# Performance work log

Hardware: AMD Instinct MI355X
Metric: run time of the kernel (lower is better)

The kernel has to match this reference:

```python
import jax, jax.numpy as jnp
import numpy as np

NUM_HEADS = 12
WIN = 7  # window_size[0] == window_size[1]


def setup_inputs() -> dict:
    key = jax.random.key(0)
    ks = jax.random.split(key, 8)
    B_, N, C = 2048, WIN * WIN, 384
    nW = 64
    return {
        "x": jax.random.normal(ks[0], (B_, N, C), dtype=jnp.float32),
        "mask": jax.random.normal(ks[1], (nW, N, N), dtype=jnp.float32),
        "qkv_w": jax.random.normal(ks[2], (3 * C, C), dtype=jnp.float32) * 0.02,
        "qkv_b": jax.random.normal(ks[3], (3 * C,), dtype=jnp.float32) * 0.02,
        "proj_w": jax.random.normal(ks[4], (C, C), dtype=jnp.float32) * 0.02,
        "proj_b": jax.random.normal(ks[5], (C,), dtype=jnp.float32) * 0.02,
        "rpb_table": jax.random.normal(ks[6], ((2 * WIN - 1) ** 2, NUM_HEADS), dtype=jnp.float32) * 0.02,
        "rel_index": jax.random.randint(ks[7], (N * N,), 0, (2 * WIN - 1) ** 2, dtype=jnp.int32),
    }


def reference(x, mask, qkv_w, qkv_b, proj_w, proj_b, rpb_table, rel_index):
    B_, N, C = x.shape
    H = NUM_HEADS
    d = C // H
    scale = d ** -0.5

    # QKV projection (quant wrappers act as identity in non-quant state)
    qkv = x @ qkv_w.T + qkv_b                      # [B_, N, 3C]
    qkv = qkv.reshape(B_, N, 3, H, d).transpose(2, 0, 3, 1, 4)  # [3, B_, H, N, d]
    q, k, v = qkv[0], qkv[1], qkv[2]

    attn = jnp.einsum("bhnd,bhmd->bhnm", q * scale, k)  # [B_, H, N, N]

    # relative position bias gather: [N*N] -> [N, N, H] -> [H, N, N]
    bias = rpb_table[rel_index].reshape(N, N, H).transpose(2, 0, 1)
    attn = attn + bias[None]

    # shifted-window mask add
    nW = mask.shape[0]
    attn = attn.reshape(B_ // nW, nW, H, N, N) + mask[None, :, None]
    attn = attn.reshape(B_, H, N, N)

    attn = jax.nn.softmax(attn, axis=-1)

    out = jnp.einsum("bhnm,bhmd->bhnd", attn, v)   # [B_, H, N, d]
    out = out.transpose(0, 2, 1, 3).reshape(B_, N, C)
    out = out @ proj_w.T + proj_b
    return out, attn
```

## Files before the change

kernel.cpp:

```cpp
#include <hip/hip_runtime.h>
#include <hip/hip_bf16.h>
#include <stdint.h>

#define H_ 12
#define D_ 32
#define N_ 49
#define C_ 384
#define B_TOT 2048
#define BH 24576
#define M_ROWS 100352
#define SCALE 0.17677669529663689f

typedef float f32x4 __attribute__((ext_vector_type(4)));
typedef __bf16 bf16x8 __attribute__((ext_vector_type(8)));
typedef unsigned short ushortx8 __attribute__((ext_vector_type(8)));

static __device__ __forceinline__ unsigned short f2bf(float f) {
  __bf16 b = (__bf16)f;
  return __builtin_bit_cast(unsigned short, b);
}

__global__ void cast_bf16(const float* __restrict__ in,
                          unsigned short* __restrict__ out, int n8) {
  int i = blockIdx.x * blockDim.x + threadIdx.x;
  const int stride = gridDim.x * blockDim.x;
  for (; i < n8; i += stride) {
    float4 a = ((const float4*)in)[2 * i];
    float4 b = ((const float4*)in)[2 * i + 1];
    ushortx8 v;
    v[0] = f2bf(a.x); v[1] = f2bf(a.y); v[2] = f2bf(a.z); v[3] = f2bf(a.w);
    v[4] = f2bf(b.x); v[5] = f2bf(b.y); v[6] = f2bf(b.z); v[7] = f2bf(b.w);
    *(ushortx8*)&out[(size_t)i * 8] = v;
  }
}

__global__ void build_comb(const float* __restrict__ mask,
                           const float* __restrict__ rpb,
                           const int* __restrict__ ridx,
                           float* __restrict__ comb) {
  const int h = blockIdx.x, w = blockIdx.y;
  float* cb = comb + (size_t)(w * H_ + h) * 4096;
  const float* mw = mask + (size_t)w * N_ * N_;
  for (int e = threadIdx.x; e < 4096; e += 256) {
    const int r = e >> 6, c = e & 63;
    float v;
    if (c >= N_) v = -1e30f;
    else if (r >= N_) v = 0.0f;
    else v = mw[r * N_ + c] + rpb[ridx[r * N_ + c] * H_ + h];
    cb[e] = v;
  }
}

__global__ __launch_bounds__(256, 3)
void qkv_gemm(const unsigned short* __restrict__ A,
              const unsigned short* __restrict__ W,
              const float* __restrict__ bias, unsigned short* __restrict__ qkv) {
  __shared__ unsigned short lA[2][128 * 40];
  __shared__ unsigned short lB[2][128 * 40];
  const int tid = threadIdx.x;
  const int bn = blockIdx.x, bm = blockIdx.y;
  const int lane = tid & 63, wv = tid >> 6;
  const int wm = wv >> 1, wn = wv & 1;
  const int lo = lane & 15, hi = lane >> 4;
  const int r0 = tid >> 2, r1 = r0 + 64;
  const int off = (tid & 3) * 8;

  const unsigned short* Ab = A + (size_t)bm * 128 * 384;
  const unsigned short* Wb = W + (size_t)bn * 128 * 384;

  f32x4 acc[4][4];
#pragma unroll
  for (int i = 0; i < 4; i++)
#pragma unroll
    for (int j = 0; j < 4; j++)
#pragma unroll
      for (int r = 0; r < 4; r++) acc[i][j][r] = 0.0f;

  *(uint4*)&lA[0][r0 * 40 + off] = *(const uint4*)(Ab + r0 * 384 + off);
  *(uint4*)&lA[0][r1 * 40 + off] = *(const uint4*)(Ab + r1 * 384 + off);
  *(uint4*)&lB[0][r0 * 40 + off] = *(const uint4*)(Wb + r0 * 384 + off);
  *(uint4*)&lB[0][r1 * 40 + off] = *(const uint4*)(Wb + r1 * 384 + off);
  __syncthreads();

  int buf = 0;
  for (int kt = 0; kt < 12; kt++) {
    uint4 pa0, pa1, pb0, pb1;
    if (kt < 11) {
      const int kc = (kt + 1) * 32 + off;
      pa0 = *(const uint4*)(Ab + r0 * 384 + kc);
      pa1 = *(const uint4*)(Ab + r1 * 384 + kc);
      pb0 = *(const uint4*)(Wb + r0 * 384 + kc);
      pb1 = *(const uint4*)(Wb + r1 * 384 + kc);
    }
    bf16x8 af[4], bfm[4];
#pragma unroll
    for (int mt = 0; mt < 4; mt++)
      af[mt] = *(const bf16x8*)&lA[buf][(wm * 64 + mt * 16 + lo) * 40 + hi * 8];
#pragma unroll
    for (int nt = 0; nt < 4; nt++)
      bfm[nt] = *(const bf16x8*)&lB[buf][(wn * 64 + nt * 16 + lo) * 40 + hi * 8];
#pragma unroll
    for (int mt = 0; mt < 4; mt++)
#pragma unroll
      for (int nt = 0; nt < 4; nt++)
        acc[mt][nt] = __builtin_amdgcn_mfma_f32_16x16x32_bf16(af[mt], bfm[nt], acc[mt][nt], 0, 0, 0);
    if (kt < 11) {
      *(uint4*)&lA[buf ^ 1][r0 * 40 + off] = pa0;
      *(uint4*)&lA[buf ^ 1][r1 * 40 + off] = pa1;
      *(uint4*)&lB[buf ^ 1][r0 * 40 + off] = pb0;
      *(uint4*)&lB[buf ^ 1][r1 * 40 + off] = pb1;
    }
    __syncthreads();
    buf ^= 1;
  }

#pragma unroll
  for (int nt = 0; nt < 4; nt++) {
    const int j = bn * 128 + wn * 64 + nt * 16 + lo;
    const float bj = bias[j];
    const int which = j / 384;
    const int rem = j - which * 384;
    const int h = rem >> 5, dd = rem & 31;
    const float mul = (which == 0) ? SCALE : 1.0f;
#pragma unroll
    for (int mt = 0; mt < 4; mt++) {
#pragma unroll
      for (int r = 0; r < 4; r++) {
        const int i = bm * 128 + wm * 64 + mt * 16 + hi * 4 + r;
        const int b = i / 49, sq = i - b * 49;
        const float val = (acc[mt][nt][r] + bj) * mul;
        qkv[((size_t)which * BH + (size_t)b * H_ + h) * (N_ * D_) + sq * D_ + dd] = f2bf(val);
      }
    }
  }
}

__global__ __launch_bounds__(64, 2)
void attn_kernel(const unsigned short* __restrict__ qkv,
                 const float* __restrict__ comb,
                 float* __restrict__ probs,
                 unsigned short* __restrict__ av) {
  __shared__ unsigned short P[64 * 72];
  __shared__ unsigned short VT[32 * 72];
  const int lane = threadIdx.x;
  const int lo = lane & 15, hi = lane >> 4;
  const int h = blockIdx.x, b = blockIdx.y;

  const unsigned short* qp = qkv + (size_t)(b * H_ + h) * (N_ * D_);
  const unsigned short* kp = qp + (size_t)BH * (N_ * D_);
  const unsigned short* vp = kp + (size_t)BH * (N_ * D_);

  {
    unsigned int* vz = (unsigned int*)VT;
#pragma unroll
    for (int i = 0; i < 18; i++) vz[lane + 64 * i] = 0u;
  }
  __syncthreads();

  bf16x8 aq[4], bk[4];
#pragma unroll
  for (int t = 0; t < 4; t++) {
    aq[t] = *(const bf16x8*)(qp + (t * 16 + lo) * D_ + hi * 8);
    bk[t] = *(const bf16x8*)(kp + (t * 16 + lo) * D_ + hi * 8);
  }
  f32x4 s[4][4];
#pragma unroll
  for (int mt = 0; mt < 4; mt++)
#pragma unroll
    for (int nt = 0; nt < 4; nt++) {
#pragma unroll
      for (int r = 0; r < 4; r++) s[mt][nt][r] = 0.0f;
      s[mt][nt] = __builtin_amdgcn_mfma_f32_16x16x32_bf16(aq[mt], bk[nt], s[mt][nt], 0, 0, 0);
    }

#pragma unroll
  for (int it = 0; it < 4; it++) {
    const int idx = it * 64 + lane;
    if (idx < 196) {
      const int sq = idx >> 2, ch = idx & 3;
      ushortx8 vv = *(const ushortx8*)(vp + sq * D_ + ch * 8);
#pragma unroll
      for (int jj = 0; jj < 8; jj++) VT[(ch * 8 + jj) * 72 + sq] = vv[jj];
    }
  }

  const float* cb = comb + (size_t)((b & 63) * H_ + h) * 4096;
#pragma unroll
  for (int mt = 0; mt < 4; mt++) {
#pragma unroll
    for (int r = 0; r < 4; r++) {
      const int row = mt * 16 + hi * 4 + r;
      const float* crow = cb + row * 64 + lo;
      float v0 = s[mt][0][r] + crow[0];
      float v1 = s[mt][1][r] + crow[16];
      float v2 = s[mt][2][r] + crow[32];
      float v3 = s[mt][3][r] + crow[48];
      float m = fmaxf(fmaxf(v0, v1), fmaxf(v2, v3));
      m = fmaxf(m, __shfl_xor(m, 1));
      m = fmaxf(m, __shfl_xor(m, 2));
      m = fmaxf(m, __shfl_xor(m, 4));
      m = fmaxf(m, __shfl_xor(m, 8));
      v0 = __expf(v0 - m); v1 = __expf(v1 - m);
      v2 = __expf(v2 - m); v3 = __expf(v3 - m);
      float sum = v0 + v1 + v2 + v3;
      sum += __shfl_xor(sum, 1);
      sum += __shfl_xor(sum, 2);
      sum += __shfl_xor(sum, 4);
      sum += __shfl_xor(sum, 8);
      const float rinv = 1.0f / sum;
      s[mt][0][r] = v0 * rinv; s[mt][1][r] = v1 * rinv;
      s[mt][2][r] = v2 * rinv; s[mt][3][r] = v3 * rinv;
    }
  }

  const size_t pbase = (size_t)(b * H_ + h) * N_ * N_;
#pragma unroll
  for (int mt = 0; mt < 4; mt++) {
#pragma unroll
    for (int r = 0; r < 4; r++) {
      const int row = mt * 16 + hi * 4 + r;
      if (row < N_) {
#pragma unroll
        for (int nt = 0; nt < 4; nt++) {
          const int c = nt * 16 + lo;
          if (c < N_) probs[pbase + row * N_ + c] = s[mt][nt][r];
        }
      }
#pragma unroll
      for (int nt = 0; nt < 4; nt++)
        P[row * 72 + nt * 16 + lo] = f2bf(s[mt][nt][r]);
    }
  }
  __syncthreads();

  f32x4 o[4][2];
#pragma unroll
  for (int mt = 0; mt < 4; mt++)
#pragma unroll
    for (int n2 = 0; n2 < 2; n2++)
#pragma unroll
      for (int r = 0; r < 4; r++) o[mt][n2][r] = 0.0f;
#pragma unroll
  for (int ks = 0; ks < 2; ks++) {
    bf16x8 pa[4], vb[2];
#pragma unroll
    for (int mt = 0; mt < 4; mt++)
      pa[mt] = *(const bf16x8*)&P[(mt * 16 + lo) * 72 + ks * 32 + hi * 8];
#pragma unroll
    for (int n2 = 0; n2 < 2; n2++)
      vb[n2] = *(const bf16x8*)&VT[(n2 * 16 + lo) * 72 + ks * 32 + hi * 8];
#pragma unroll
    for (int mt = 0; mt < 4; mt++)
#pragma unroll
      for (int n2 = 0; n2 < 2; n2++)
        o[mt][n2] = __builtin_amdgcn_mfma_f32_16x16x32_bf16(pa[mt], vb[n2], o[mt][n2], 0, 0, 0);
  }

#pragma unroll
  for (int mt = 0; mt < 4; mt++) {
#pragma unroll
    for (int r = 0; r < 4; r++) {
      const int row = mt * 16 + hi * 4 + r;
      if (row < N_) {
#pragma unroll
        for (int n2 = 0; n2 < 2; n2++) {
          const int dv = n2 * 16 + lo;
          av[((size_t)b * N_ + row) * C_ + h * D_ + dv] = f2bf(o[mt][n2][r]);
        }
      }
    }
  }
}

__global__ __launch_bounds__(256, 3)
void proj_gemm(const unsigned short* __restrict__ A,
               const unsigned short* __restrict__ W,
               const float* __restrict__ bias, float* __restrict__ out) {
  __shared__ unsigned short lA[2][128 * 40];
  __shared__ unsigned short lB[2][128 * 40];
  const int tid = threadIdx.x;
  const int bn = blockIdx.x, bm = blockIdx.y;
  const int lane = tid & 63, wv = tid >> 6;
  const int wm = wv >> 1, wn = wv & 1;
  const int lo = lane & 15, hi = lane >> 4;
  const int r0 = tid >> 2, r1 = r0 + 64;
  const int off = (tid & 3) * 8;

  const unsigned short* Ab = A + (size_t)bm * 128 * 384;
  const unsigned short* Wb = W + (size_t)bn * 128 * 384;

  f32x4 acc[4][4];
#pragma unroll
  for (int i = 0; i < 4; i++)
#pragma unroll
    for (int j = 0; j < 4; j++)
#pragma unroll
      for (int r = 0; r < 4; r++) acc[i][j][r] = 0.0f;

  *(uint4*)&lA[0][r0 * 40 + off] = *(const uint4*)(Ab + r0 * 384 + off);
  *(uint4*)&lA[0][r1 * 40 + off] = *(const uint4*)(Ab + r1 * 384 + off);
  *(uint4*)&lB[0][r0 * 40 + off] = *(const uint4*)(Wb + r0 * 384 + off);
  *(uint4*)&lB[0][r1 * 40 + off] = *(const uint4*)(Wb + r1 * 384 + off);
  __syncthreads();

  int buf = 0;
  for (int kt = 0; kt < 12; kt++) {
    uint4 pa0, pa1, pb0, pb1;
    if (kt < 11) {
      const int kc = (kt + 1) * 32 + off;
      pa0 = *(const uint4*)(Ab + r0 * 384 + kc);
      pa1 = *(const uint4*)(Ab + r1 * 384 + kc);
      pb0 = *(const uint4*)(Wb + r0 * 384 + kc);
      pb1 = *(const uint4*)(Wb + r1 * 384 + kc);
    }
    bf16x8 af[4], bfm[4];
#pragma unroll
    for (int mt = 0; mt < 4; mt++)
      af[mt] = *(const bf16x8*)&lA[buf][(wm * 64 + mt * 16 + lo) * 40 + hi * 8];
#pragma unroll
    for (int nt = 0; nt < 4; nt++)
      bfm[nt] = *(const bf16x8*)&lB[buf][(wn * 64 + nt * 16 + lo) * 40 + hi * 8];
#pragma unroll
    for (int mt = 0; mt < 4; mt++)
#pragma unroll
      for (int nt = 0; nt < 4; nt++)
        acc[mt][nt] = __builtin_amdgcn_mfma_f32_16x16x32_bf16(af[mt], bfm[nt], acc[mt][nt], 0, 0, 0);
    if (kt < 11) {
      *(uint4*)&lA[buf ^ 1][r0 * 40 + off] = pa0;
      *(uint4*)&lA[buf ^ 1][r1 * 40 + off] = pa1;
      *(uint4*)&lB[buf ^ 1][r0 * 40 + off] = pb0;
      *(uint4*)&lB[buf ^ 1][r1 * 40 + off] = pb1;
    }
    __syncthreads();
    buf ^= 1;
  }

#pragma unroll
  for (int nt = 0; nt < 4; nt++) {
    const int j = bn * 128 + wn * 64 + nt * 16 + lo;
    const float bj = bias[j];
#pragma unroll
    for (int mt = 0; mt < 4; mt++) {
#pragma unroll
      for (int r = 0; r < 4; r++) {
        const int i = bm * 128 + wm * 64 + mt * 16 + hi * 4 + r;
        out[(size_t)i * 384 + j] = acc[mt][nt][r] + bj;
      }
    }
  }
}

extern "C" void kernel_launch(void* const* d_in, const int* in_sizes, int n_in,
                              void* d_out, int out_size, void* d_ws, size_t ws_size,
                              hipStream_t stream) {
  const float* x      = (const float*)d_in[0];
  const float* mask   = (const float*)d_in[1];
  const float* qkv_w  = (const float*)d_in[2];
  const float* qkv_b  = (const float*)d_in[3];
  const float* proj_w = (const float*)d_in[4];
  const float* proj_b = (const float*)d_in[5];
  const float* rpb    = (const float*)d_in[6];
  const int*   ridx   = (const int*)d_in[7];

  unsigned short* qkv   = (unsigned short*)d_ws;
  unsigned short* av    = qkv + (size_t)3 * BH * N_ * D_;
  unsigned short* x_bf  = av;
  float* comb           = (float*)(av + (size_t)M_ROWS * C_);
  unsigned short* wq_bf = (unsigned short*)(comb + 768 * 4096);
  unsigned short* wp_bf = wq_bf + 1152 * 384;
  float* out   = (float*)d_out;
  float* probs = out + (size_t)M_ROWS * C_;

  cast_bf16<<<2048, 256, 0, stream>>>(x, x_bf, M_ROWS * C_ / 8);
  cast_bf16<<<216, 256, 0, stream>>>(qkv_w, wq_bf, 1152 * 384 / 8);
  cast_bf16<<<72, 256, 0, stream>>>(proj_w, wp_bf, 384 * 384 / 8);
  build_comb<<<dim3(H_, 64), 256, 0, stream>>>(mask, rpb, ridx, comb);
  qkv_gemm<<<dim3(9, 784), 256, 0, stream>>>(x_bf, wq_bf, qkv_b, qkv);
  attn_kernel<<<dim3(H_, B_TOT), 64, 0, stream>>>(qkv, comb, probs, av);
  proj_gemm<<<dim3(3, 784), 256, 0, stream>>>(av, wp_bf, proj_b, out);
}
```

Before: 557.2 us.

## Stage GEMM and attention epilogues through LDS for vectorized stores; remap block order

```diff
diff --git a/kernel.cpp b/kernel.cpp
--- a/kernel.cpp
+++ b/kernel.cpp
@@ -55,10 +55,14 @@
 void qkv_gemm(const unsigned short* __restrict__ A,
               const unsigned short* __restrict__ W,
               const float* __restrict__ bias, unsigned short* __restrict__ qkv) {
-  __shared__ unsigned short lA[2][128 * 40];
-  __shared__ unsigned short lB[2][128 * 40];
+  __shared__ __align__(16) unsigned short smem[20480];
+  unsigned short* lA0 = smem;
+  unsigned short* lB0 = smem + 10240;
   const int tid = threadIdx.x;
-  const int bn = blockIdx.x, bm = blockIdx.y;
+  const int w = blockIdx.x;
+  const int t = (w & 7) * 882 + (w >> 3);
+  const int bm = t / 9, bn = t - bm * 9;
+
   const int lane = tid & 63, wv = tid >> 6;
   const int wm = wv >> 1, wn = wv & 1;
   const int lo = lane & 15, hi = lane >> 4;
@@ -76,10 +80,10 @@
 #pragma unroll
       for (int r = 0; r < 4; r++) acc[i][j][r] = 0.0f;
 
-  *(uint4*)&lA[0][r0 * 40 + off] = *(const uint4*)(Ab + r0 * 384 + off);
-  *(uint4*)&lA[0][r1 * 40 + off] = *(const uint4*)(Ab + r1 * 384 + off);
-  *(uint4*)&lB[0][r0 * 40 + off] = *(const uint4*)(Wb + r0 * 384 + off);
-  *(uint4*)&lB[0][r1 * 40 + off] = *(const uint4*)(Wb + r1 * 384 + off);
+  *(uint4*)&lA0[r0 * 40 + off] = *(const uint4*)(Ab + r0 * 384 + off);
+  *(uint4*)&lA0[r1 * 40 + off] = *(const uint4*)(Ab + r1 * 384 + off);
+  *(uint4*)&lB0[r0 * 40 + off] = *(const uint4*)(Wb + r0 * 384 + off);
+  *(uint4*)&lB0[r1 * 40 + off] = *(const uint4*)(Wb + r1 * 384 + off);
   __syncthreads();
 
   int buf = 0;
@@ -92,46 +96,64 @@
       pb0 = *(const uint4*)(Wb + r0 * 384 + kc);
       pb1 = *(const uint4*)(Wb + r1 * 384 + kc);
     }
+    const unsigned short* la = lA0 + buf * 5120;
+    const unsigned short* lb = lB0 + buf * 5120;
     bf16x8 af[4], bfm[4];
 #pragma unroll
     for (int mt = 0; mt < 4; mt++)
-      af[mt] = *(const bf16x8*)&lA[buf][(wm * 64 + mt * 16 + lo) * 40 + hi * 8];
+      af[mt] = *(const bf16x8*)&la[(wm * 64 + mt * 16 + lo) * 40 + hi * 8];
 #pragma unroll
     for (int nt = 0; nt < 4; nt++)
-      bfm[nt] = *(const bf16x8*)&lB[buf][(wn * 64 + nt * 16 + lo) * 40 + hi * 8];
+      bfm[nt] = *(const bf16x8*)&lb[(wn * 64 + nt * 16 + lo) * 40 + hi * 8];
 #pragma unroll
     for (int mt = 0; mt < 4; mt++)
 #pragma unroll
       for (int nt = 0; nt < 4; nt++)
         acc[mt][nt] = __builtin_amdgcn_mfma_f32_16x16x32_bf16(af[mt], bfm[nt], acc[mt][nt], 0, 0, 0);
     if (kt < 11) {
-      *(uint4*)&lA[buf ^ 1][r0 * 40 + off] = pa0;
-      *(uint4*)&lA[buf ^ 1][r1 * 40 + off] = pa1;
-      *(uint4*)&lB[buf ^ 1][r0 * 40 + off] = pb0;
-      *(uint4*)&lB[buf ^ 1][r1 * 40 + off] = pb1;
+      unsigned short* wa = lA0 + (buf ^ 1) * 5120;
+      unsigned short* wb = lB0 + (buf ^ 1) * 5120;
+      *(uint4*)&wa[r0 * 40 + off] = pa0;
+      *(uint4*)&wa[r1 * 40 + off] = pa1;
+      *(uint4*)&wb[r0 * 40 + off] = pb0;
+      *(uint4*)&wb[r1 * 40 + off] = pb1;
     }
     __syncthreads();
     buf ^= 1;
   }
 
+  unsigned short* ep = smem + wv * 5120;
 #pragma unroll
   for (int nt = 0; nt < 4; nt++) {
     const int j = bn * 128 + wn * 64 + nt * 16 + lo;
     const float bj = bias[j];
-    const int which = j / 384;
-    const int rem = j - which * 384;
-    const int h = rem >> 5, dd = rem & 31;
-    const float mul = (which == 0) ? SCALE : 1.0f;
+    const float mul = (j < 384) ? SCALE : 1.0f;
+    const int ch = nt >> 1;
+    const int dd = (nt & 1) * 16 + lo;
 #pragma unroll
     for (int mt = 0; mt < 4; mt++) {
 #pragma unroll
       for (int r = 0; r < 4; r++) {
-        const int i = bm * 128 + wm * 64 + mt * 16 + hi * 4 + r;
-        const int b = i / 49, sq = i - b * 49;
-        const float val = (acc[mt][nt][r] + bj) * mul;
-        qkv[((size_t)which * BH + (size_t)b * H_ + h) * (N_ * D_) + sq * D_ + dd] = f2bf(val);
+        const int row = mt * 16 + hi * 4 + r;
+        ep[(row * 2 + ch) * 40 + dd] = f2bf((acc[mt][nt][r] + bj) * mul);
       }
     }
+  }
+#pragma unroll
+  for (int cc = 0; cc < 2; cc++) {
+    const int cidx = cc * 64 + lane;
+    const int lr = cidx >> 1, lch = cidx & 1;
+    const int i = bm * 128 + wm * 64 + lr;
+    const int b = i / 49, sq = i - b * 49;
+    const int j0 = bn * 128 + wn * 64 + lch * 32;
+    const int which = j0 / 384;
+    const int rem = j0 - which * 384;
+    const int h = rem >> 5;
+    unsigned short* dst = qkv + ((size_t)which * BH + (size_t)b * H_ + h) * (N_ * D_) + sq * D_;
+    const unsigned short* src = ep + cidx * 40;
+#pragma unroll
+    for (int q = 0; q < 4; q++)
+      *(uint4*)(dst + q * 8) = *(const uint4*)(src + q * 8);
   }
 }
 
@@ -140,8 +162,8 @@
                  const float* __restrict__ comb,
                  float* __restrict__ probs,
                  unsigned short* __restrict__ av) {
-  __shared__ unsigned short P[64 * 72];
-  __shared__ unsigned short VT[32 * 72];
+  __shared__ __align__(16) unsigned short P[64 * 72];
+  __shared__ __align__(16) unsigned short VT[32 * 72];
   const int lane = threadIdx.x;
   const int lo = lane & 15, hi = lane >> 4;
   const int h = blockIdx.x, b = blockIdx.y;
@@ -256,6 +278,7 @@
         o[mt][n2] = __builtin_amdgcn_mfma_f32_16x16x32_bf16(pa[mt], vb[n2], o[mt][n2], 0, 0, 0);
   }
 
+  __syncthreads();
 #pragma unroll
   for (int mt = 0; mt < 4; mt++) {
 #pragma unroll
@@ -263,12 +286,17 @@
       const int row = mt * 16 + hi * 4 + r;
       if (row < N_) {
 #pragma unroll
-        for (int n2 = 0; n2 < 2; n2++) {
-          const int dv = n2 * 16 + lo;
-          av[((size_t)b * N_ + row) * C_ + h * D_ + dv] = f2bf(o[mt][n2][r]);
-        }
+        for (int n2 = 0; n2 < 2; n2++)
+          P[row * 40 + n2 * 16 + lo] = f2bf(o[mt][n2][r]);
       }
     }
+  }
+  if (lane < N_) {
+    unsigned short* dst = av + ((size_t)b * N_ + lane) * C_ + h * D_;
+    const unsigned short* src = P + lane * 40;
+#pragma unroll
+    for (int q = 0; q < 4; q++)
+      *(uint4*)(dst + q * 8) = *(const uint4*)(src + q * 8);
   }
 }
 
@@ -279,7 +307,9 @@
   __shared__ unsigned short lA[2][128 * 40];
   __shared__ unsigned short lB[2][128 * 40];
   const int tid = threadIdx.x;
-  const int bn = blockIdx.x, bm = blockIdx.y;
+  const int w = blockIdx.x;
+  const int t = (w & 7) * 294 + (w >> 3);
+  const int bm = t / 3, bn = t - bm * 3;
   const int lane = tid & 63, wv = tid >> 6;
   const int wm = wv >> 1, wn = wv & 1;
   const int lo = lane & 15, hi = lane >> 4;
@@ -375,7 +405,7 @@
   cast_bf16<<<216, 256, 0, stream>>>(qkv_w, wq_bf, 1152 * 384 / 8);
   cast_bf16<<<72, 256, 0, stream>>>(proj_w, wp_bf, 384 * 384 / 8);
   build_comb<<<dim3(H_, 64), 256, 0, stream>>>(mask, rpb, ridx, comb);
-  qkv_gemm<<<dim3(9, 784), 256, 0, stream>>>(x_bf, wq_bf, qkv_b, qkv);
+  qkv_gemm<<<7056, 256, 0, stream>>>(x_bf, wq_bf, qkv_b, qkv);
   attn_kernel<<<dim3(H_, B_TOT), 64, 0, stream>>>(qkv, comb, probs, av);
-  proj_gemm<<<dim3(3, 784), 256, 0, stream>>>(av, wp_bf, proj_b, out);
-}
+  proj_gemm<<<2352, 256, 0, stream>>>(av, wp_bf, proj_b, out);
+}
```

Result: faster. 480.3 us (-13.8%).
